# Kernel tuning notes

Hardware: AMD Instinct MI355X
Metric: run time of the kernel (lower is better)

The kernel has to match this reference:

```python
import jax, jax.numpy as jnp
import numpy as np

NUM_GRAPHS = 128

def setup_inputs() -> dict:
    key = jax.random.key(0)
    ks = jax.random.split(key, 12)
    N, E = 50000, 800000
    x = jax.random.normal(ks[0], (N, 54), dtype=jnp.float32)
    edge_index = jax.random.randint(ks[1], (2, E), 0, N, dtype=jnp.int64)
    batch = jnp.sort(jax.random.randint(ks[2], (N,), 0, NUM_GRAPHS, dtype=jnp.int64))
    def lin(k, fi, fo):
        return jax.random.normal(k, (fi, fo), dtype=jnp.float32) / np.sqrt(fi)
    return {
        "x": x, "edge_index": edge_index, "batch": batch,
        "W1l": lin(ks[3], 54, 128), "b1": jnp.zeros((128,), jnp.float32), "W1r": lin(ks[4], 54, 128),
        "W2l": lin(ks[5], 128, 256), "b2": jnp.zeros((256,), jnp.float32), "W2r": lin(ks[6], 128, 256),
        "W3l": lin(ks[7], 256, 256), "b3": jnp.zeros((256,), jnp.float32), "W3r": lin(ks[8], 256, 256),
    }

def _sage(h, src, dst, n, Wl, b, Wr):
    # sum-aggregate neighbor features x_j (j=src) into node i (i=dst), then
    # out = lin_l(agg) + lin_r(h)  (PyG SAGEConv, aggr='sum')
    agg = jax.ops.segment_sum(h[src], dst, num_segments=n)
    return jax.nn.relu(agg @ Wl + b + h @ Wr)

def reference(x, edge_index, batch, W1l, b1, W1r, W2l, b2, W2r, W3l, b3, W3r):
    n = x.shape[0]
    src, dst = edge_index[0], edge_index[1]
    h = _sage(x, src, dst, n, W1l, b1, W1r)
    h = _sage(h, src, dst, n, W2l, b2, W2r)
    h = _sage(h, src, dst, n, W3l, b3, W3r)
    # global mean pool per graph (gep = global_mean_pool)
    sums = jax.ops.segment_sum(h, batch, num_segments=NUM_GRAPHS)
    cnts = jax.ops.segment_sum(jnp.ones((n, 1), h.dtype), batch, num_segments=NUM_GRAPHS)
    return sums / jnp.maximum(cnts, 1.0)
```

## Files before the change

### kernel.cpp

```cpp
#include <hip/hip_runtime.h>


typedef unsigned short u16;
typedef __attribute__((ext_vector_type(8))) short bf16x8;
typedef __attribute__((ext_vector_type(4))) float f32x4;

__device__ __forceinline__ u16 f2b(float f) {
    union { float f; unsigned u; } v; v.f = f;
    unsigned u = v.u;
    return (u16)((u + 0x7FFF + ((u >> 16) & 1)) >> 16);
}
__device__ __forceinline__ float b2f(u16 h) {
    union { unsigned u; float f; } v; v.u = ((unsigned)h) << 16;
    return v.f;
}
__device__ __forceinline__ float blo(unsigned u) {
    union { unsigned u; float f; } v; v.u = u << 16;
    return v.f;
}
__device__ __forceinline__ float bhi(unsigned u) {
    union { unsigned u; float f; } v; v.u = u & 0xffff0000u;
    return v.f;
}

__global__ void k_prep(const float* __restrict__ x,
                       const float* __restrict__ W1l, const float* __restrict__ W1r,
                       const float* __restrict__ W2l, const float* __restrict__ W2r,
                       const float* __restrict__ W3l, const float* __restrict__ W3r,
                       u16* __restrict__ xb,
                       u16* __restrict__ wt1l, u16* __restrict__ wt1r,
                       u16* __restrict__ wt2l, u16* __restrict__ wt2r,
                       u16* __restrict__ wt3l, u16* __restrict__ wt3r, int N) {
    long idx = (long)blockIdx.x * 256 + threadIdx.x;
    long s0 = (long)N * 54;
    if (idx < s0) { xb[idx] = f2b(x[idx]); return; }
    idx -= s0;
    if (idx < 2 * 128 * 64) {
        u16* o = (idx < 128 * 64) ? wt1l : wt1r;
        const float* w = (idx < 128 * 64) ? W1l : W1r;
        long loc = idx % (128 * 64);
        int d = (int)(loc >> 6), k = (int)(loc & 63);
        o[loc] = (k < 54) ? f2b(w[(long)k * 128 + d]) : 0;
        return;
    }
    idx -= 2 * 128 * 64;
    if (idx < 2 * 256 * 128) {
        u16* o = (idx < 256 * 128) ? wt2l : wt2r;
        const float* w = (idx < 256 * 128) ? W2l : W2r;
        long loc = idx % (256 * 128);
        int d = (int)(loc >> 7), k = (int)(loc & 127);
        o[loc] = f2b(w[(long)k * 256 + d]);
        return;
    }
    idx -= 2 * 256 * 128;
    if (idx < 2 * 256 * 256) {
        u16* o = (idx < 256 * 256) ? wt3l : wt3r;
        const float* w = (idx < 256 * 256) ? W3l : W3r;
        long loc = idx % (256 * 256);
        int d = (int)(loc >> 8), k = (int)(loc & 255);
        o[loc] = f2b(w[(long)k * 256 + d]);
    }
}

__global__ void k_count(const int* __restrict__ dst, int* __restrict__ cnt, int E) {
    int e = blockIdx.x * 256 + threadIdx.x;
    if (e < E) atomicAdd(&cnt[dst[e]], 1);
}

__global__ void k_bsum(const int* __restrict__ cnt, int* __restrict__ bsum, int N) {
    __shared__ int sm[256];
    int i = blockIdx.x * 256 + threadIdx.x;
    sm[threadIdx.x] = (i < N) ? cnt[i] : 0;
    __syncthreads();
    for (int off = 128; off > 0; off >>= 1) {
        if (threadIdx.x < off) sm[threadIdx.x] += sm[threadIdx.x + off];
        __syncthreads();
    }
    if (threadIdx.x == 0) bsum[blockIdx.x] = sm[0];
}

__global__ void k_bscan(const int* __restrict__ bsum, int* __restrict__ boff, int NB) {
    __shared__ int sm[256];
    int t = threadIdx.x;
    int v = (t < NB) ? bsum[t] : 0;
    sm[t] = v;
    __syncthreads();
    for (int off = 1; off < 256; off <<= 1) {
        int add = (t >= off) ? sm[t - off] : 0;
        __syncthreads();
        sm[t] += add;
        __syncthreads();
    }
    if (t < NB) boff[t] = sm[t] - v;
}

__global__ void k_scan(const int* __restrict__ cnt, const int* __restrict__ boff,
                       int* __restrict__ rowptr, int* __restrict__ wpos, int N, int E) {
    __shared__ int sm[256];
    int t = threadIdx.x;
    int i = blockIdx.x * 256 + t;
    int v = (i < N) ? cnt[i] : 0;
    sm[t] = v;
    __syncthreads();
    for (int off = 1; off < 256; off <<= 1) {
        int add = (t >= off) ? sm[t - off] : 0;
        __syncthreads();
        sm[t] += add;
        __syncthreads();
    }
    int ex = sm[t] - v + boff[blockIdx.x];
    if (i < N) { rowptr[i] = ex; wpos[i] = ex; }
    if (i == 0) rowptr[N] = E;
}

__global__ void k_fill(const int* __restrict__ src, const int* __restrict__ dst,
                       int* __restrict__ wpos, int* __restrict__ csr, int E) {
    int e = blockIdx.x * 256 + threadIdx.x;
    if (e < E) {
        int p = atomicAdd(&wpos[dst[e]], 1);
        csr[p] = src[e];
    }
}

__global__ __launch_bounds__(256) void k_agg54(const u16* __restrict__ h,
                                               const int* __restrict__ rowptr,
                                               const int* __restrict__ csr,
                                               u16* __restrict__ agg, int n) {
    constexpr int D = 54;
    int w = threadIdx.x >> 6;
    int lane = threadIdx.x & 63;
    int i = blockIdx.x * 4 + w;
    if (i >= n) return;
    int b0 = rowptr[i], b1 = rowptr[i + 1];
    if (lane < D) {
        float a0 = 0.f;
        #pragma unroll 8
        for (int b = b0; b < b1; ++b) {
            int s = csr[b];
            a0 += b2f(h[(size_t)s * D + lane]);
        }
        agg[(size_t)i * D + lane] = f2b(a0);
    }
}

template <int D, int EPW>
__global__ __launch_bounds__(256) void k_aggv(const u16* __restrict__ h,
                                              const int* __restrict__ rowptr,
                                              const int* __restrict__ csr,
                                              u16* __restrict__ agg, int n) {
    constexpr int GRP = 64 / EPW;
    static_assert(D == GRP * 8, "geometry");
    int w = threadIdx.x >> 6;
    int lane = threadIdx.x & 63;
    int i = blockIdx.x * 4 + w;
    if (i >= n) return;
    int b0 = rowptr[i], b1 = rowptr[i + 1];
    int sub = lane / GRP;
    int dl = lane % GRP;

    float a0 = 0.f, a1 = 0.f, a2 = 0.f, a3 = 0.f;
    float a4 = 0.f, a5 = 0.f, a6 = 0.f, a7 = 0.f;

    int b = b0;
    #pragma unroll 4
    for (; b + EPW <= b1; b += EPW) {
        int s = csr[b + sub];
        uint4 v = *reinterpret_cast<const uint4*>(h + (size_t)s * D + dl * 8);
        a0 += blo(v.x); a1 += bhi(v.x);
        a2 += blo(v.y); a3 += bhi(v.y);
        a4 += blo(v.z); a5 += bhi(v.z);
        a6 += blo(v.w); a7 += bhi(v.w);
    }
    int rem = b1 - b;
    if (sub < rem) {
        int s = csr[b + sub];
        uint4 v = *reinterpret_cast<const uint4*>(h + (size_t)s * D + dl * 8);
        a0 += blo(v.x); a1 += bhi(v.x);
        a2 += blo(v.y); a3 += bhi(v.y);
        a4 += blo(v.z); a5 += bhi(v.z);
        a6 += blo(v.w); a7 += bhi(v.w);
    }
    #pragma unroll
    for (int off = GRP; off < 64; off <<= 1) {
        a0 += __shfl_xor(a0, off, 64);
        a1 += __shfl_xor(a1, off, 64);
        a2 += __shfl_xor(a2, off, 64);
        a3 += __shfl_xor(a3, off, 64);
        a4 += __shfl_xor(a4, off, 64);
        a5 += __shfl_xor(a5, off, 64);
        a6 += __shfl_xor(a6, off, 64);
        a7 += __shfl_xor(a7, off, 64);
    }
    if (sub == 0) {
        uint4 o;
        o.x = ((unsigned)f2b(a0)) | (((unsigned)f2b(a1)) << 16);
        o.y = ((unsigned)f2b(a2)) | (((unsigned)f2b(a3)) << 16);
        o.z = ((unsigned)f2b(a4)) | (((unsigned)f2b(a5)) << 16);
        o.w = ((unsigned)f2b(a6)) | (((unsigned)f2b(a7)) << 16);
        *reinterpret_cast<uint4*>(agg + (size_t)i * D + dl * 8) = o;
    }
}

template <int KA, int KW, int DOUT, bool A16>
__global__ __launch_bounds__(256) void k_mgemm(const u16* __restrict__ A1,
                                               const u16* __restrict__ A2,
                                               const u16* __restrict__ Wt1,
                                               const u16* __restrict__ Wt2,
                                               const float* __restrict__ bias,
                                               u16* __restrict__ C, int N) {
    constexpr int BM = 128, BKP = 40;
    __shared__ u16 As[BM * BKP];
    __shared__ u16 Bs[BM * BKP];

    const int tid = threadIdx.x;
    const int w = tid >> 6, l = tid & 63;
    const int wr = w >> 1, wc = w & 1;
    const int lo = l & 15, hi = l >> 4;
    const int m0 = blockIdx.x * BM;
    const int n0 = blockIdx.y * 128;

    f32x4 acc[4][4];
    #pragma unroll
    for (int i = 0; i < 4; ++i)
        #pragma unroll
        for (int j = 0; j < 4; ++j) acc[i][j] = {0.f, 0.f, 0.f, 0.f};

    constexpr int KT = KW / 32;

    #pragma unroll
    for (int s = 0; s < 2; ++s) {
        const u16* __restrict__ Ap = s ? A2 : A1;
        const u16* __restrict__ Wp = s ? Wt2 : Wt1;
        for (int kt = 0; kt < KT; ++kt) {
            const int k0 = kt * 32;
            #pragma unroll
            for (int it = 0; it < 2; ++it) {
                int v = it * 256 + tid;
                int r = v >> 2, c = v & 3;
                uint4 val = *reinterpret_cast<const uint4*>(Wp + (size_t)(n0 + r) * KW + k0 + c * 8);
                *reinterpret_cast<uint4*>(&Bs[r * BKP + c * 8]) = val;
            }
            if constexpr (A16) {
                #pragma unroll
                for (int it = 0; it < 2; ++it) {
                    int v = it * 256 + tid;
                    int r = v >> 2, c = v & 3;
                    int m = m0 + r;
                    uint4 val = {0u, 0u, 0u, 0u};
                    if (m < N) val = *reinterpret_cast<const uint4*>(Ap + (size_t)m * KA + k0 + c * 8);
                    *reinterpret_cast<uint4*>(&As[r * BKP + c * 8]) = val;
                }
            } else {
                #pragma unroll
                for (int it = 0; it < 8; ++it) {
                    int v = it * 256 + tid;
                    int r = v >> 4, c = v & 15;
                    int m = m0 + r;
                    int k = k0 + c * 2;
                    unsigned val = 0;
                    if (m < N && k < KA)
                        val = *reinterpret_cast<const unsigned*>(Ap + (size_t)m * KA + k);
                    *reinterpret_cast<unsigned*>(&As[r * BKP + c * 2]) = val;
                }
            }
            __syncthreads();
            bf16x8 af[4], bf[4];
            #pragma unroll
            for (int f = 0; f < 4; ++f) {
                af[f] = *reinterpret_cast<const bf16x8*>(&Bs[(wc * 64 + f * 16 + lo) * BKP + hi * 8]);
                bf[f] = *reinterpret_cast<const bf16x8*>(&As[(wr * 64 + f * 16 + lo) * BKP + hi * 8]);
            }
            #pragma unroll
            for (int fm = 0; fm < 4; ++fm)
                #pragma unroll
                for (int fn = 0; fn < 4; ++fn)
                    acc[fm][fn] = __builtin_amdgcn_mfma_f32_16x16x32_bf16(af[fn], bf[fm], acc[fm][fn], 0, 0, 0);
            __syncthreads();
        }
    }
    #pragma unroll
    for (int fm = 0; fm < 4; ++fm) {
        int node = m0 + wr * 64 + fm * 16 + lo;
        if (node < N) {
            #pragma unroll
            for (int fn = 0; fn < 4; ++fn) {
                int fb = n0 + wc * 64 + fn * 16 + hi * 4;
                float4 bv = *reinterpret_cast<const float4*>(bias + fb);
                ushort4 o;
                o.x = f2b(fmaxf(acc[fm][fn][0] + bv.x, 0.f));
                o.y = f2b(fmaxf(acc[fm][fn][1] + bv.y, 0.f));
                o.z = f2b(fmaxf(acc[fm][fn][2] + bv.z, 0.f));
                o.w = f2b(fmaxf(acc[fm][fn][3] + bv.w, 0.f));
                *reinterpret_cast<ushort4*>(C + (size_t)node * DOUT + fb) = o;
            }
        }
    }
}

template <int ROWS>
__global__ void k_pool(const u16* __restrict__ h3, const int* __restrict__ batch,
                       float* __restrict__ outsum, int* __restrict__ cnt, int N) {
    int r0 = blockIdx.x * ROWS;
    int r1 = min(r0 + ROWS, N);
    if (r0 >= N) return;
    int d = threadIdx.x;
    int cur = batch[r0];
    float s = 0.f;
    int c = 0;
    for (int i = r0; i < r1; ++i) {
        int g = batch[i];
        if (g != cur) {
            atomicAdd(&outsum[cur * 256 + d], s);
            if (d == 0) atomicAdd(&cnt[cur], c);
            s = 0.f; c = 0; cur = g;
        }
        s += b2f(h3[(size_t)i * 256 + d]);
        c++;
    }
    atomicAdd(&outsum[cur * 256 + d], s);
    if (d == 0) atomicAdd(&cnt[cur], c);
}

__global__ void k_div(float* __restrict__ out, const int* __restrict__ cnt, int total) {
    int idx = blockIdx.x * 256 + threadIdx.x;
    if (idx < total) {
        float c = fmaxf((float)cnt[idx >> 8], 1.0f);
        out[idx] = out[idx] / c;
    }
}

extern "C" void kernel_launch(void* const* d_in, const int* in_sizes, int n_in,
                              void* d_out, int out_size, void* d_ws, size_t ws_size,
                              hipStream_t stream) {
    const float* x   = (const float*)d_in[0];
    const int* ei    = (const int*)d_in[1];
    const int* batch = (const int*)d_in[2];
    const float* W1l = (const float*)d_in[3];
    const float* b1  = (const float*)d_in[4];
    const float* W1r = (const float*)d_in[5];
    const float* W2l = (const float*)d_in[6];
    const float* b2  = (const float*)d_in[7];
    const float* W2r = (const float*)d_in[8];
    const float* W3l = (const float*)d_in[9];
    const float* b3  = (const float*)d_in[10];
    const float* W3r = (const float*)d_in[11];

    const int N = in_sizes[0] / 54;
    const int E = in_sizes[1] / 2;
    const int* src = ei;
    const int* dst = ei + E;

    u16* xb   = (u16*)d_ws;
    u16* bufA = xb + (size_t)N * 54;
    u16* buf1 = bufA + (size_t)N * 256;
    u16* buf2 = buf1 + (size_t)N * 256;
    u16* wt1l = buf2 + (size_t)N * 256;
    u16* wt1r = wt1l + 128 * 64;
    u16* wt2l = wt1r + 128 * 64;
    u16* wt2r = wt2l + 256 * 128;
    u16* wt3l = wt2r + 256 * 128;
    u16* wt3r = wt3l + 256 * 256;
    int* ip = (int*)(wt3r + 256 * 256);
    int* cntdeg  = ip; ip += N;
    int* rowptr  = ip; ip += N + 1;
    int* wpos    = ip; ip += N + 1;
    int* bsum    = ip; ip += 256;
    int* boff    = ip; ip += 256;
    int* cntpool = ip; ip += 128;
    int* csr     = ip;

    hipMemsetAsync(cntdeg, 0, (size_t)N * sizeof(int), stream);
    hipMemsetAsync(d_out, 0, (size_t)out_size * sizeof(float), stream);
    hipMemsetAsync(cntpool, 0, 128 * sizeof(int), stream);

    const int NB = (N + 255) / 256;
    const int EB = (E + 255) / 256;

    {
        long total = (long)N * 54 + 2L * 128 * 64 + 2L * 256 * 128 + 2L * 256 * 256;
        int g = (int)((total + 255) / 256);
        k_prep<<<g, 256, 0, stream>>>(x, W1l, W1r, W2l, W2r, W3l, W3r,
                                      xb, wt1l, wt1r, wt2l, wt2r, wt3l, wt3r, N);
    }

    k_count<<<EB, 256, 0, stream>>>(dst, cntdeg, E);
    k_bsum<<<NB, 256, 0, stream>>>(cntdeg, bsum, N);
    k_bscan<<<1, 256, 0, stream>>>(bsum, boff, NB);
    k_scan<<<NB, 256, 0, stream>>>(cntdeg, boff, rowptr, wpos, N, E);
    k_fill<<<EB, 256, 0, stream>>>(src, dst, wpos, csr, E);

    const int AGB = (N + 3) / 4;
    const int GX = (N + 127) / 128;

    k_agg54<<<AGB, 256, 0, stream>>>(xb, rowptr, csr, bufA, N);
    {
        dim3 g(GX, 1);
        k_mgemm<54, 64, 128, false><<<g, 256, 0, stream>>>(bufA, xb, wt1l, wt1r, b1, buf1, N);
    }
    k_aggv<128, 4><<<AGB, 256, 0, stream>>>(buf1, rowptr, csr, bufA, N);
    {
        dim3 g(GX, 2);
        k_mgemm<128, 128, 256, true><<<g, 256, 0, stream>>>(bufA, buf1, wt2l, wt2r, b2, buf2, N);
    }
    k_aggv<256, 2><<<AGB, 256, 0, stream>>>(buf2, rowptr, csr, bufA, N);
    {
        dim3 g(GX, 2);
        k_mgemm<256, 256, 256, true><<<g, 256, 0, stream>>>(bufA, buf2, wt3l, wt3r, b3, buf1, N);
    }

    k_pool<32><<<(N + 31) / 32, 256, 0, stream>>>(buf1, batch, (float*)d_out, cntpool, N);
    k_div<<<(out_size + 255) / 256, 256, 0, stream>>>((float*)d_out, cntpool, out_size);
}
```

Measured before the change: 349.5 us.

## Fuse neighbor aggregation into SAGE GEMM kernel keeping aggregates in LDS

Each SAGE layer now runs as a single kernel. The kernel gathers neighbor sums for a 64-node tile into shared memory, then runs the MFMA GEMM over the full output width for both the aggregate and self terms. This drops the global write and reread of the aggregate buffer and three kernel launches per forward. In exchange, the gather and GEMM phases no longer overlap across kernels, blocks use more LDS, and the 512-thread blocks serialize eight nodes per wave during the gather.

```diff
diff --git a/kernel.cpp b/kernel.cpp
--- a/kernel.cpp
+++ b/kernel.cpp
@@ -122,169 +122,149 @@
     }
 }
 
-__global__ __launch_bounds__(256) void k_agg54(const u16* __restrict__ h,
+template <int KA, int KW, int DOUT, int EPW>
+__global__ __launch_bounds__(512) void k_fused(const u16* __restrict__ h,
                                                const int* __restrict__ rowptr,
                                                const int* __restrict__ csr,
-                                               u16* __restrict__ agg, int n) {
-    constexpr int D = 54;
-    int w = threadIdx.x >> 6;
-    int lane = threadIdx.x & 63;
-    int i = blockIdx.x * 4 + w;
-    if (i >= n) return;
-    int b0 = rowptr[i], b1 = rowptr[i + 1];
-    if (lane < D) {
-        float a0 = 0.f;
-        #pragma unroll 8
-        for (int b = b0; b < b1; ++b) {
-            int s = csr[b];
-            a0 += b2f(h[(size_t)s * D + lane]);
-        }
-        agg[(size_t)i * D + lane] = f2b(a0);
-    }
-}
-
-template <int D, int EPW>
-__global__ __launch_bounds__(256) void k_aggv(const u16* __restrict__ h,
-                                              const int* __restrict__ rowptr,
-                                              const int* __restrict__ csr,
-                                              u16* __restrict__ agg, int n) {
-    constexpr int GRP = 64 / EPW;
-    static_assert(D == GRP * 8, "geometry");
-    int w = threadIdx.x >> 6;
-    int lane = threadIdx.x & 63;
-    int i = blockIdx.x * 4 + w;
-    if (i >= n) return;
-    int b0 = rowptr[i], b1 = rowptr[i + 1];
-    int sub = lane / GRP;
-    int dl = lane % GRP;
-
-    float a0 = 0.f, a1 = 0.f, a2 = 0.f, a3 = 0.f;
-    float a4 = 0.f, a5 = 0.f, a6 = 0.f, a7 = 0.f;
-
-    int b = b0;
-    #pragma unroll 4
-    for (; b + EPW <= b1; b += EPW) {
-        int s = csr[b + sub];
-        uint4 v = *reinterpret_cast<const uint4*>(h + (size_t)s * D + dl * 8);
-        a0 += blo(v.x); a1 += bhi(v.x);
-        a2 += blo(v.y); a3 += bhi(v.y);
-        a4 += blo(v.z); a5 += bhi(v.z);
-        a6 += blo(v.w); a7 += bhi(v.w);
-    }
-    int rem = b1 - b;
-    if (sub < rem) {
-        int s = csr[b + sub];
-        uint4 v = *reinterpret_cast<const uint4*>(h + (size_t)s * D + dl * 8);
-        a0 += blo(v.x); a1 += bhi(v.x);
-        a2 += blo(v.y); a3 += bhi(v.y);
-        a4 += blo(v.z); a5 += bhi(v.z);
-        a6 += blo(v.w); a7 += bhi(v.w);
-    }
-    #pragma unroll
-    for (int off = GRP; off < 64; off <<= 1) {
-        a0 += __shfl_xor(a0, off, 64);
-        a1 += __shfl_xor(a1, off, 64);
-        a2 += __shfl_xor(a2, off, 64);
-        a3 += __shfl_xor(a3, off, 64);
-        a4 += __shfl_xor(a4, off, 64);
-        a5 += __shfl_xor(a5, off, 64);
-        a6 += __shfl_xor(a6, off, 64);
-        a7 += __shfl_xor(a7, off, 64);
-    }
-    if (sub == 0) {
-        uint4 o;
-        o.x = ((unsigned)f2b(a0)) | (((unsigned)f2b(a1)) << 16);
-        o.y = ((unsigned)f2b(a2)) | (((unsigned)f2b(a3)) << 16);
-        o.z = ((unsigned)f2b(a4)) | (((unsigned)f2b(a5)) << 16);
-        o.w = ((unsigned)f2b(a6)) | (((unsigned)f2b(a7)) << 16);
-        *reinterpret_cast<uint4*>(agg + (size_t)i * D + dl * 8) = o;
-    }
-}
-
-template <int KA, int KW, int DOUT, bool A16>
-__global__ __launch_bounds__(256) void k_mgemm(const u16* __restrict__ A1,
-                                               const u16* __restrict__ A2,
                                                const u16* __restrict__ Wt1,
                                                const u16* __restrict__ Wt2,
                                                const float* __restrict__ bias,
                                                u16* __restrict__ C, int N) {
-    constexpr int BM = 128, BKP = 40;
-    __shared__ u16 As[BM * BKP];
-    __shared__ u16 Bs[BM * BKP];
+    constexpr int KAP = KW + 8;
+    constexpr int WCOL = DOUT / 4;
+    constexpr int FN = WCOL / 16;
+    __shared__ u16 aggL[64 * KAP];
+    __shared__ u16 xL[(KA == 54) ? 64 * KAP : 8];
+    __shared__ u16 Bs[DOUT * 40];
 
     const int tid = threadIdx.x;
-    const int w = tid >> 6, l = tid & 63;
-    const int wr = w >> 1, wc = w & 1;
-    const int lo = l & 15, hi = l >> 4;
-    const int m0 = blockIdx.x * BM;
-    const int n0 = blockIdx.y * 128;
-
-    f32x4 acc[4][4];
+    const int w = tid >> 6, lane = tid & 63;
+    const int m0 = blockIdx.x * 64;
+
+    for (int t = 0; t < 8; ++t) {
+        int r = w * 8 + t;
+        int node = m0 + r;
+        if constexpr (KA == 54) {
+            u16 xv = 0;
+            if (node < N && lane < 54) xv = h[(size_t)node * 54 + lane];
+            xL[r * KAP + lane] = xv;
+            float a = 0.f;
+            if (node < N && lane < 54) {
+                int b0 = rowptr[node], b1 = rowptr[node + 1];
+                #pragma unroll 8
+                for (int b = b0; b < b1; ++b)
+                    a += b2f(h[(size_t)csr[b] * 54 + lane]);
+            }
+            aggL[r * KAP + lane] = f2b(a);
+        } else {
+            constexpr int GRP = 64 / EPW;
+            static_assert(KA == GRP * 8, "geometry");
+            int sub = lane / GRP, dl = lane % GRP;
+            float a0 = 0.f, a1 = 0.f, a2 = 0.f, a3 = 0.f;
+            float a4 = 0.f, a5 = 0.f, a6 = 0.f, a7 = 0.f;
+            if (node < N) {
+                int b0 = rowptr[node], b1 = rowptr[node + 1];
+                int b = b0;
+                #pragma unroll 4
+                for (; b + EPW <= b1; b += EPW) {
+                    int s = csr[b + sub];
+                    uint4 v = *reinterpret_cast<const uint4*>(h + (size_t)s * KA + dl * 8);
+                    a0 += blo(v.x); a1 += bhi(v.x);
+                    a2 += blo(v.y); a3 += bhi(v.y);
+                    a4 += blo(v.z); a5 += bhi(v.z);
+                    a6 += blo(v.w); a7 += bhi(v.w);
+                }
+                int rem = b1 - b;
+                if (sub < rem) {
+                    int s = csr[b + sub];
+                    uint4 v = *reinterpret_cast<const uint4*>(h + (size_t)s * KA + dl * 8);
+                    a0 += blo(v.x); a1 += bhi(v.x);
+                    a2 += blo(v.y); a3 += bhi(v.y);
+                    a4 += blo(v.z); a5 += bhi(v.z);
+                    a6 += blo(v.w); a7 += bhi(v.w);
+                }
+            }
+            #pragma unroll
+            for (int off = GRP; off < 64; off <<= 1) {
+                a0 += __shfl_xor(a0, off, 64);
+                a1 += __shfl_xor(a1, off, 64);
+                a2 += __shfl_xor(a2, off, 64);
+                a3 += __shfl_xor(a3, off, 64);
+                a4 += __shfl_xor(a4, off, 64);
+                a5 += __shfl_xor(a5, off, 64);
+                a6 += __shfl_xor(a6, off, 64);
+                a7 += __shfl_xor(a7, off, 64);
+            }
+            if (sub == 0) {
+                uint4 o;
+                o.x = ((unsigned)f2b(a0)) | (((unsigned)f2b(a1)) << 16);
+                o.y = ((unsigned)f2b(a2)) | (((unsigned)f2b(a3)) << 16);
+                o.z = ((unsigned)f2b(a4)) | (((unsigned)f2b(a5)) << 16);
+                o.w = ((unsigned)f2b(a6)) | (((unsigned)f2b(a7)) << 16);
+                *reinterpret_cast<uint4*>(&aggL[r * KAP + dl * 8]) = o;
+            }
+        }
+    }
+    __syncthreads();
+
+    const int wr = w >> 2, wc = w & 3;
+    const int lo = lane & 15, hi = lane >> 4;
+
+    f32x4 acc[2][FN];
     #pragma unroll
-    for (int i = 0; i < 4; ++i)
+    for (int i = 0; i < 2; ++i)
         #pragma unroll
-        for (int j = 0; j < 4; ++j) acc[i][j] = {0.f, 0.f, 0.f, 0.f};
+        for (int j = 0; j < FN; ++j) acc[i][j] = {0.f, 0.f, 0.f, 0.f};
 
     constexpr int KT = KW / 32;
 
     #pragma unroll
     for (int s = 0; s < 2; ++s) {
-        const u16* __restrict__ Ap = s ? A2 : A1;
         const u16* __restrict__ Wp = s ? Wt2 : Wt1;
         for (int kt = 0; kt < KT; ++kt) {
             const int k0 = kt * 32;
             #pragma unroll
-            for (int it = 0; it < 2; ++it) {
-                int v = it * 256 + tid;
+            for (int it = 0; it < DOUT / 128; ++it) {
+                int v = it * 512 + tid;
                 int r = v >> 2, c = v & 3;
-                uint4 val = *reinterpret_cast<const uint4*>(Wp + (size_t)(n0 + r) * KW + k0 + c * 8);
-                *reinterpret_cast<uint4*>(&Bs[r * BKP + c * 8]) = val;
-            }
-            if constexpr (A16) {
+                uint4 val = *reinterpret_cast<const uint4*>(Wp + (size_t)r * KW + k0 + c * 8);
+                *reinterpret_cast<uint4*>(&Bs[r * 40 + c * 8]) = val;
+            }
+            __syncthreads();
+            bf16x8 bfr[2];
+            if (s == 0) {
                 #pragma unroll
-                for (int it = 0; it < 2; ++it) {
-                    int v = it * 256 + tid;
-                    int r = v >> 2, c = v & 3;
-                    int m = m0 + r;
-                    uint4 val = {0u, 0u, 0u, 0u};
-                    if (m < N) val = *reinterpret_cast<const uint4*>(Ap + (size_t)m * KA + k0 + c * 8);
-                    *reinterpret_cast<uint4*>(&As[r * BKP + c * 8]) = val;
-                }
+                for (int fm = 0; fm < 2; ++fm)
+                    bfr[fm] = *reinterpret_cast<const bf16x8*>(&aggL[(wr * 32 + fm * 16 + lo) * KAP + k0 + hi * 8]);
+            } else if constexpr (KA == 54) {
+                #pragma unroll
+                for (int fm = 0; fm < 2; ++fm)
+                    bfr[fm] = *reinterpret_cast<const bf16x8*>(&xL[(wr * 32 + fm * 16 + lo) * KAP + k0 + hi * 8]);
             } else {
                 #pragma unroll
-                for (int it = 0; it < 8; ++it) {
-                    int v = it * 256 + tid;
-                    int r = v >> 4, c = v & 15;
-                    int m = m0 + r;
-                    int k = k0 + c * 2;
-                    unsigned val = 0;
-                    if (m < N && k < KA)
-                        val = *reinterpret_cast<const unsigned*>(Ap + (size_t)m * KA + k);
-                    *reinterpret_cast<unsigned*>(&As[r * BKP + c * 2]) = val;
+                for (int fm = 0; fm < 2; ++fm) {
+                    int m = m0 + wr * 32 + fm * 16 + lo;
+                    bf16x8 z = {0, 0, 0, 0, 0, 0, 0, 0};
+                    bfr[fm] = (m < N) ? *reinterpret_cast<const bf16x8*>(h + (size_t)m * KA + k0 + hi * 8) : z;
                 }
             }
-            __syncthreads();
-            bf16x8 af[4], bf[4];
             #pragma unroll
-            for (int f = 0; f < 4; ++f) {
-                af[f] = *reinterpret_cast<const bf16x8*>(&Bs[(wc * 64 + f * 16 + lo) * BKP + hi * 8]);
-                bf[f] = *reinterpret_cast<const bf16x8*>(&As[(wr * 64 + f * 16 + lo) * BKP + hi * 8]);
-            }
-            #pragma unroll
-            for (int fm = 0; fm < 4; ++fm)
+            for (int fn = 0; fn < FN; ++fn) {
+                bf16x8 af = *reinterpret_cast<const bf16x8*>(&Bs[(wc * WCOL + fn * 16 + lo) * 40 + hi * 8]);
                 #pragma unroll
-                for (int fn = 0; fn < 4; ++fn)
-                    acc[fm][fn] = __builtin_amdgcn_mfma_f32_16x16x32_bf16(af[fn], bf[fm], acc[fm][fn], 0, 0, 0);
+                for (int fm = 0; fm < 2; ++fm)
+                    acc[fm][fn] = __builtin_amdgcn_mfma_f32_16x16x32_bf16(af, bfr[fm], acc[fm][fn], 0, 0, 0);
+            }
             __syncthreads();
         }
     }
     #pragma unroll
-    for (int fm = 0; fm < 4; ++fm) {
-        int node = m0 + wr * 64 + fm * 16 + lo;
+    for (int fm = 0; fm < 2; ++fm) {
+        int node = m0 + wr * 32 + fm * 16 + lo;
         if (node < N) {
             #pragma unroll
-            for (int fn = 0; fn < 4; ++fn) {
-                int fb = n0 + wc * 64 + fn * 16 + hi * 4;
+            for (int fn = 0; fn < FN; ++fn) {
+                int fb = wc * WCOL + fn * 16 + hi * 4;
                 float4 bv = *reinterpret_cast<const float4*>(bias + fb);
                 ushort4 o;
                 o.x = f2b(fmaxf(acc[fm][fn][0] + bv.x, 0.f));
@@ -351,8 +331,7 @@
     const int* dst = ei + E;
 
     u16* xb   = (u16*)d_ws;
-    u16* bufA = xb + (size_t)N * 54;
-    u16* buf1 = bufA + (size_t)N * 256;
+    u16* buf1 = xb + (size_t)N * 54;
     u16* buf2 = buf1 + (size_t)N * 256;
     u16* wt1l = buf2 + (size_t)N * 256;
     u16* wt1r = wt1l + 128 * 64;
@@ -389,24 +368,11 @@
     k_scan<<<NB, 256, 0, stream>>>(cntdeg, boff, rowptr, wpos, N, E);
     k_fill<<<EB, 256, 0, stream>>>(src, dst, wpos, csr, E);
 
-    const int AGB = (N + 3) / 4;
-    const int GX = (N + 127) / 128;
-
-    k_agg54<<<AGB, 256, 0, stream>>>(xb, rowptr, csr, bufA, N);
-    {
-        dim3 g(GX, 1);
-        k_mgemm<54, 64, 128, false><<<g, 256, 0, stream>>>(bufA, xb, wt1l, wt1r, b1, buf1, N);
-    }
-    k_aggv<128, 4><<<AGB, 256, 0, stream>>>(buf1, rowptr, csr, bufA, N);
-    {
-        dim3 g(GX, 2);
-        k_mgemm<128, 128, 256, true><<<g, 256, 0, stream>>>(bufA, buf1, wt2l, wt2r, b2, buf2, N);
-    }
-    k_aggv<256, 2><<<AGB, 256, 0, stream>>>(buf2, rowptr, csr, bufA, N);
-    {
-        dim3 g(GX, 2);
-        k_mgemm<256, 256, 256, true><<<g, 256, 0, stream>>>(bufA, buf2, wt3l, wt3r, b3, buf1, N);
-    }
+    const int GB = (N + 63) / 64;
+
+    k_fused<54, 64, 128, 1><<<GB, 512, 0, stream>>>(xb, rowptr, csr, wt1l, wt1r, b1, buf1, N);
+    k_fused<128, 128, 256, 4><<<GB, 512, 0, stream>>>(buf1, rowptr, csr, wt2l, wt2r, b2, buf2, N);
+    k_fused<256, 256, 256, 2><<<GB, 512, 0, stream>>>(buf2, rowptr, csr, wt3l, wt3r, b3, buf1, N);
 
     k_pool<32><<<(N + 31) / 32, 256, 0, stream>>>(buf1, batch, (float*)d_out, cntpool, N);
     k_div<<<(out_size + 255) / 256, 256, 0, stream>>>((float*)d_out, cntpool, out_size);
```

Result: slower. 365.0 us (+4.4%).

## Use full-width 64-row GEMM tiles for 256-output SAGE layers

Applied to the files above, without the earlier changes.

Adds a 512-thread GEMM kernel that computes all 256 output columns for a 64-row node tile, replacing the previous 128x128 tiling that split output columns across two grid columns. Each block loads its activation rows once instead of twice, which removes the duplicate A reads of the column-split grid, and it launches more, smaller blocks over N. In exchange every block reloads the full weight tile per k-step into a larger shared buffer, and the old kernel is pinned to n0=0 because it is now only used for the 128-wide layer.

```diff
diff --git a/kernel.cpp b/kernel.cpp
--- a/kernel.cpp
+++ b/kernel.cpp
@@ -217,7 +217,7 @@
     const int wr = w >> 1, wc = w & 1;
     const int lo = l & 15, hi = l >> 4;
     const int m0 = blockIdx.x * BM;
-    const int n0 = blockIdx.y * 128;
+    const int n0 = 0;
 
     f32x4 acc[4][4];
     #pragma unroll
@@ -297,6 +297,87 @@
     }
 }
 
+template <int KA, int DOUT>
+__global__ __launch_bounds__(512) void k_mgemm2(const u16* __restrict__ A1,
+                                                const u16* __restrict__ A2,
+                                                const u16* __restrict__ Wt1,
+                                                const u16* __restrict__ Wt2,
+                                                const float* __restrict__ bias,
+                                                u16* __restrict__ C, int N) {
+    constexpr int BM = 64, BKP = 40;
+    constexpr int WCOL = DOUT / 4;
+    constexpr int FN = WCOL / 16;
+    __shared__ u16 As[BM * BKP];
+    __shared__ u16 Bs[DOUT * BKP];
+
+    const int tid = threadIdx.x;
+    const int w = tid >> 6, lane = tid & 63;
+    const int wr = w >> 2, wc = w & 3;
+    const int lo = lane & 15, hi = lane >> 4;
+    const int m0 = blockIdx.x * BM;
+
+    f32x4 acc[2][FN];
+    #pragma unroll
+    for (int i = 0; i < 2; ++i)
+        #pragma unroll
+        for (int j = 0; j < FN; ++j) acc[i][j] = {0.f, 0.f, 0.f, 0.f};
+
+    constexpr int KT = KA / 32;
+
+    #pragma unroll
+    for (int s = 0; s < 2; ++s) {
+        const u16* __restrict__ Ap = s ? A2 : A1;
+        const u16* __restrict__ Wp = s ? Wt2 : Wt1;
+        for (int kt = 0; kt < KT; ++kt) {
+            const int k0 = kt * 32;
+            #pragma unroll
+            for (int it = 0; it < DOUT * 32 / 8 / 512; ++it) {
+                int v = it * 512 + tid;
+                int r = v >> 2, c = v & 3;
+                uint4 val = *reinterpret_cast<const uint4*>(Wp + (size_t)r * KA + k0 + c * 8);
+                *reinterpret_cast<uint4*>(&Bs[r * BKP + c * 8]) = val;
+            }
+            if (tid < 256) {
+                int r = tid >> 2, c = tid & 3;
+                int m = m0 + r;
+                uint4 val = {0u, 0u, 0u, 0u};
+                if (m < N) val = *reinterpret_cast<const uint4*>(Ap + (size_t)m * KA + k0 + c * 8);
+                *reinterpret_cast<uint4*>(&As[r * BKP + c * 8]) = val;
+            }
+            __syncthreads();
+            bf16x8 bfr[2];
+            #pragma unroll
+            for (int fm = 0; fm < 2; ++fm)
+                bfr[fm] = *reinterpret_cast<const bf16x8*>(&As[(wr * 32 + fm * 16 + lo) * BKP + hi * 8]);
+            #pragma unroll
+            for (int fn = 0; fn < FN; ++fn) {
+                bf16x8 af = *reinterpret_cast<const bf16x8*>(&Bs[(wc * WCOL + fn * 16 + lo) * BKP + hi * 8]);
+                #pragma unroll
+                for (int fm = 0; fm < 2; ++fm)
+                    acc[fm][fn] = __builtin_amdgcn_mfma_f32_16x16x32_bf16(af, bfr[fm], acc[fm][fn], 0, 0, 0);
+            }
+            __syncthreads();
+        }
+    }
+    #pragma unroll
+    for (int fm = 0; fm < 2; ++fm) {
+        int node = m0 + wr * 32 + fm * 16 + lo;
+        if (node < N) {
+            #pragma unroll
+            for (int fn = 0; fn < FN; ++fn) {
+                int fb = wc * WCOL + fn * 16 + hi * 4;
+                float4 bv = *reinterpret_cast<const float4*>(bias + fb);
+                ushort4 o;
+                o.x = f2b(fmaxf(acc[fm][fn][0] + bv.x, 0.f));
+                o.y = f2b(fmaxf(acc[fm][fn][1] + bv.y, 0.f));
+                o.z = f2b(fmaxf(acc[fm][fn][2] + bv.z, 0.f));
+                o.w = f2b(fmaxf(acc[fm][fn][3] + bv.w, 0.f));
+                *reinterpret_cast<ushort4*>(C + (size_t)node * DOUT + fb) = o;
+            }
+        }
+    }
+}
+
 template <int ROWS>
 __global__ void k_pool(const u16* __restrict__ h3, const int* __restrict__ batch,
                        float* __restrict__ outsum, int* __restrict__ cnt, int N) {
@@ -391,22 +472,14 @@
 
     const int AGB = (N + 3) / 4;
     const int GX = (N + 127) / 128;
+    const int GX2 = (N + 63) / 64;
 
     k_agg54<<<AGB, 256, 0, stream>>>(xb, rowptr, csr, bufA, N);
-    {
-        dim3 g(GX, 1);
-        k_mgemm<54, 64, 128, false><<<g, 256, 0, stream>>>(bufA, xb, wt1l, wt1r, b1, buf1, N);
-    }
+    k_mgemm<54, 64, 128, false><<<GX, 256, 0, stream>>>(bufA, xb, wt1l, wt1r, b1, buf1, N);
     k_aggv<128, 4><<<AGB, 256, 0, stream>>>(buf1, rowptr, csr, bufA, N);
-    {
-        dim3 g(GX, 2);
-        k_mgemm<128, 128, 256, true><<<g, 256, 0, stream>>>(bufA, buf1, wt2l, wt2r, b2, buf2, N);
-    }
+    k_mgemm2<128, 256><<<GX2, 512, 0, stream>>>(bufA, buf1, wt2l, wt2r, b2, buf2, N);
     k_aggv<256, 2><<<AGB, 256, 0, stream>>>(buf2, rowptr, csr, bufA, N);
-    {
-        dim3 g(GX, 2);
-        k_mgemm<256, 256, 256, true><<<g, 256, 0, stream>>>(bufA, buf2, wt3l, wt3r, b3, buf1, N);
-    }
+    k_mgemm2<256, 256><<<GX2, 512, 0, stream>>>(bufA, buf2, wt3l, wt3r, b3, buf1, N);
 
     k_pool<32><<<(N + 31) / 32, 256, 0, stream>>>(buf1, batch, (float*)d_out, cntpool, N);
     k_div<<<(out_size + 255) / 256, 256, 0, stream>>>((float*)d_out, cntpool, out_size);
```

Result: no change. 342.9 us (-1.9%).
